# Performance work log

Hardware: AMD Instinct MI355X
Metric: run time of the kernel (lower is better)

Reference implementation:

```python
import jax, jax.numpy as jnp
import numpy as np

N_VOXELS = 400_000
FEAT_DIM = 128
BATCH = 4
NY = 512
NX = 512


def setup_inputs() -> dict:
    key = jax.random.key(0)
    k_feat, k_b, k_y, k_x = jax.random.split(key, 4)
    voxel_feat = jax.random.normal(k_feat, (N_VOXELS, FEAT_DIM), dtype=jnp.float32)
    b = jax.random.randint(k_b, (N_VOXELS,), 0, BATCH, dtype=jnp.int64 if jax.config.jax_enable_x64 else jnp.int32)
    z = jnp.zeros((N_VOXELS,), dtype=b.dtype)
    y = jax.random.randint(k_y, (N_VOXELS,), 0, NY, dtype=b.dtype)
    x = jax.random.randint(k_x, (N_VOXELS,), 0, NX, dtype=b.dtype)
    coors = jnp.stack([b, z, y, x], axis=1)  # [N, 4] = (batch, z, y, x)
    return {"voxel_feat": voxel_feat, "coors": coors, "batch_size": BATCH, "ny": NY, "nx": NX}


def reference(voxel_feat, coors, batch_size, ny, nx):
    # Fused equivalent of the per-batch python loop in _window2bev_old:
    # one flat scatter into a [B*ny*nx, C] canvas, then reshape to BEV layout.
    feat_dim = voxel_feat.shape[-1]
    flat_idx = coors[:, 0] * (ny * nx) + coors[:, 2] * nx + coors[:, 3]  # [N]
    canvas = jnp.zeros((batch_size * ny * nx, feat_dim), dtype=voxel_feat.dtype)
    canvas = canvas.at[flat_idx].set(voxel_feat)
    # [B, ny, nx, C] -> [B, C, ny, nx] to match torch output
    return canvas.reshape(batch_size, ny, nx, feat_dim).transpose(0, 3, 1, 2)
```

## Files before the change

kernel.cpp:

```cpp
#include <hip/hip_runtime.h>

#define FEAT_C 128
#define NB     4
#define NYv    512
#define NXv    512

typedef float vfloat4 __attribute__((ext_vector_type(4)));

__global__ void scatter_ids(const int4* __restrict__ coors,
                            int* __restrict__ idx_map, int n) {
    int i = blockIdx.x * blockDim.x + threadIdx.x;
    if (i >= n) return;
    int4 c = coors[i];
    int flat = c.x * (NYv * NXv) + c.z * NXv + c.w;
    atomicMax(&idx_map[flat], i);
}

__global__ __launch_bounds__(256) void gather_bev(
        const float* __restrict__ feat,
        const int* __restrict__ idx_map,
        float* __restrict__ out) {
    __shared__ float tile[64 * FEAT_C];
    __shared__ int sv[64];

    const int bid  = blockIdx.x;
    const int xseg = bid & 7;
    const int y    = (bid >> 3) & (NYv - 1);
    const int b    = bid >> (3 + 9);
    const int tid  = threadIdx.x;

    const int pix_base = b * (NYv * NXv) + y * NXv + xseg * 64;
    if (tid < 64) sv[tid] = idx_map[pix_base + tid];
    __syncthreads();

    const int wave = tid >> 6;
    const int lane = tid & 63;
    const int half = lane >> 5;
    const int l    = lane & 31;
#pragma unroll
    for (int k = 0; k < 8; ++k) {
        const int p = wave * 16 + 2 * k + half;
        const int v = sv[p];
        vfloat4 f = {0.f, 0.f, 0.f, 0.f};
        if (v >= 0) {
            f = ((const vfloat4*)(feat + v * FEAT_C))[l];
        }
        const int sw   = 4 * ((p >> 2) & 7);
        const int word = p * FEAT_C + ((4 * l) ^ sw);
        *(vfloat4*)&tile[word] = f;
    }
    __syncthreads();

    const long plane = (long)NYv * NXv;
    float* out_base = out + (long)b * FEAT_C * plane + (long)y * NXv + xseg * 64;
#pragma unroll
    for (int it = 0; it < 8; ++it) {
        const int j  = it * 256 + tid;
        const int c  = j >> 4;
        const int m  = j & 15;
        const int i0 = m << 2;
        const int cs = c ^ (4 * (m & 7));
        vfloat4 r;
        r.x = tile[(i0 + 0) * FEAT_C + cs];
        r.y = tile[(i0 + 1) * FEAT_C + cs];
        r.z = tile[(i0 + 2) * FEAT_C + cs];
        r.w = tile[(i0 + 3) * FEAT_C + cs];
        __builtin_nontemporal_store(r, (vfloat4*)(out_base + (long)c * plane + i0));
    }
}

extern "C" void kernel_launch(void* const* d_in, const int* in_sizes, int n_in,
                              void* d_out, int out_size, void* d_ws, size_t ws_size,
                              hipStream_t stream) {
    const float* feat  = (const float*)d_in[0];
    const int*   coors = (const int*)d_in[1];
    const int n = in_sizes[1] / 4;

    int* idx_map = (int*)d_ws;
    const size_t map_bytes = (size_t)NB * NYv * NXv * sizeof(int);

    (void)hipMemsetAsync(idx_map, 0xFF, map_bytes, stream);

    scatter_ids<<<(n + 255) / 256, 256, 0, stream>>>(
        (const int4*)coors, idx_map, n);

    const int nblocks = NB * NYv * (NXv / 64);
    gather_bev<<<nblocks, 256, 0, stream>>>(feat, idx_map, (float*)d_out);
}
```

Before: 707.6 us.

## Retile BEV gather to full-row by 32-channel blocks, drop nontemporal stores

Each block now covers a full 512-pixel row for a 32-channel group instead of a 64-pixel segment across all 128 channels. Threads read 128-byte slices of each voxel feature row, and each output channel row is written as one contiguous 2KB run. Nontemporal stores are replaced by regular stores. Each feature row is now fetched by four different blocks, so the feature read pattern is more fragmented in exchange for longer contiguous writes.

```diff
diff --git a/kernel.cpp b/kernel.cpp
--- a/kernel.cpp
+++ b/kernel.cpp
@@ -4,6 +4,8 @@
 #define NB     4
 #define NYv    512
 #define NXv    512
+#define CG     32
+#define NCG    (FEAT_C / CG)
 
 typedef float vfloat4 __attribute__((ext_vector_type(4)));
 
@@ -16,56 +18,54 @@
     atomicMax(&idx_map[flat], i);
 }
 
-__global__ __launch_bounds__(256) void gather_bev(
+__global__ __launch_bounds__(512) void gather_bev(
         const float* __restrict__ feat,
         const int* __restrict__ idx_map,
         float* __restrict__ out) {
-    __shared__ float tile[64 * FEAT_C];
-    __shared__ int sv[64];
+    __shared__ float tile[NXv * CG];
+    __shared__ int sv[NXv];
 
-    const int bid  = blockIdx.x;
-    const int xseg = bid & 7;
-    const int y    = (bid >> 3) & (NYv - 1);
-    const int b    = bid >> (3 + 9);
-    const int tid  = threadIdx.x;
+    const int bid = blockIdx.x;
+    const int cg  = bid & (NCG - 1);
+    const int y   = (bid >> 2) & (NYv - 1);
+    const int b   = bid >> 11;
+    const int tid = threadIdx.x;
 
-    const int pix_base = b * (NYv * NXv) + y * NXv + xseg * 64;
-    if (tid < 64) sv[tid] = idx_map[pix_base + tid];
+    sv[tid] = idx_map[b * (NYv * NXv) + y * NXv + tid];
     __syncthreads();
 
     const int wave = tid >> 6;
     const int lane = tid & 63;
-    const int half = lane >> 5;
-    const int l    = lane & 31;
+    const int sub  = lane >> 3;
+    const int l8   = lane & 7;
 #pragma unroll
     for (int k = 0; k < 8; ++k) {
-        const int p = wave * 16 + 2 * k + half;
+        const int p = wave * 64 + k * 8 + sub;
         const int v = sv[p];
         vfloat4 f = {0.f, 0.f, 0.f, 0.f};
         if (v >= 0) {
-            f = ((const vfloat4*)(feat + v * FEAT_C))[l];
+            f = ((const vfloat4*)(feat + (size_t)v * FEAT_C + cg * CG))[l8];
         }
-        const int sw   = 4 * ((p >> 2) & 7);
-        const int word = p * FEAT_C + ((4 * l) ^ sw);
+        const int word = p * CG + ((4 * l8) ^ (4 * ((p >> 2) & 7)));
         *(vfloat4*)&tile[word] = f;
     }
     __syncthreads();
 
     const long plane = (long)NYv * NXv;
-    float* out_base = out + (long)b * FEAT_C * plane + (long)y * NXv + xseg * 64;
+    float* out_base = out + ((long)b * FEAT_C + cg * CG) * plane + (long)y * NXv;
 #pragma unroll
     for (int it = 0; it < 8; ++it) {
-        const int j  = it * 256 + tid;
-        const int c  = j >> 4;
-        const int m  = j & 15;
+        const int j  = it * 512 + tid;
+        const int c  = ((j >> 4) & 3) + 4 * (j >> 9);
+        const int m  = (j & 15) + 16 * ((j >> 6) & 7);
         const int i0 = m << 2;
         const int cs = c ^ (4 * (m & 7));
         vfloat4 r;
-        r.x = tile[(i0 + 0) * FEAT_C + cs];
-        r.y = tile[(i0 + 1) * FEAT_C + cs];
-        r.z = tile[(i0 + 2) * FEAT_C + cs];
-        r.w = tile[(i0 + 3) * FEAT_C + cs];
-        __builtin_nontemporal_store(r, (vfloat4*)(out_base + (long)c * plane + i0));
+        r.x = tile[(i0 + 0) * CG + cs];
+        r.y = tile[(i0 + 1) * CG + cs];
+        r.z = tile[(i0 + 2) * CG + cs];
+        r.w = tile[(i0 + 3) * CG + cs];
+        *(vfloat4*)(out_base + (long)c * plane + i0) = r;
     }
 }
 
@@ -84,6 +84,6 @@
     scatter_ids<<<(n + 255) / 256, 256, 0, stream>>>(
         (const int4*)coors, idx_map, n);
 
-    const int nblocks = NB * NYv * (NXv / 64);
-    gather_bev<<<nblocks, 256, 0, stream>>>(feat, idx_map, (float*)d_out);
+    const int nblocks = NB * NYv * NCG;
+    gather_bev<<<nblocks, 512, 0, stream>>>(feat, idx_map, (float*)d_out);
 }
```

Measured after the change: 742.1 us. 4.9% more time.

## Widen gather tile to 256 pixels per block with 1024 threads

Applied to the files above, without the earlier changes.

The gather/transpose kernel now handles 256 consecutive x pixels per block using 1024 threads and a 128KB shared-memory tile, instead of 64 pixels with 256 threads. The output write mapping is reorganized so each half-wave stores one channel across 128 contiguous pixels, producing longer contiguous row segments per channel in the NCHW output. The larger tile limits occupancy to about one block per CU because of LDS usage, and there are 4x fewer blocks.

```diff
diff --git a/kernel.cpp b/kernel.cpp
--- a/kernel.cpp
+++ b/kernel.cpp
@@ -4,6 +4,7 @@
 #define NB     4
 #define NYv    512
 #define NXv    512
+#define PX     256
 
 typedef float vfloat4 __attribute__((ext_vector_type(4)));
 
@@ -16,50 +17,50 @@
     atomicMax(&idx_map[flat], i);
 }
 
-__global__ __launch_bounds__(256) void gather_bev(
+__global__ __launch_bounds__(1024) void gather_bev(
         const float* __restrict__ feat,
         const int* __restrict__ idx_map,
         float* __restrict__ out) {
-    __shared__ float tile[64 * FEAT_C];
-    __shared__ int sv[64];
+    __shared__ float tile[PX * FEAT_C];
+    __shared__ int sv[PX];
 
-    const int bid  = blockIdx.x;
-    const int xseg = bid & 7;
-    const int y    = (bid >> 3) & (NYv - 1);
-    const int b    = bid >> (3 + 9);
-    const int tid  = threadIdx.x;
+    const int bid = blockIdx.x;
+    const int xh  = bid & 1;
+    const int y   = (bid >> 1) & (NYv - 1);
+    const int b   = bid >> 10;
+    const int tid = threadIdx.x;
 
-    const int pix_base = b * (NYv * NXv) + y * NXv + xseg * 64;
-    if (tid < 64) sv[tid] = idx_map[pix_base + tid];
+    if (tid < PX)
+        sv[tid] = idx_map[b * (NYv * NXv) + y * NXv + xh * PX + tid];
     __syncthreads();
 
     const int wave = tid >> 6;
     const int lane = tid & 63;
     const int half = lane >> 5;
     const int l    = lane & 31;
+    const int hw   = wave * 2 + half;
 #pragma unroll
     for (int k = 0; k < 8; ++k) {
-        const int p = wave * 16 + 2 * k + half;
+        const int p = hw * 8 + k;
         const int v = sv[p];
         vfloat4 f = {0.f, 0.f, 0.f, 0.f};
         if (v >= 0) {
-            f = ((const vfloat4*)(feat + v * FEAT_C))[l];
+            f = ((const vfloat4*)(feat + (size_t)v * FEAT_C))[l];
         }
-        const int sw   = 4 * ((p >> 2) & 7);
-        const int word = p * FEAT_C + ((4 * l) ^ sw);
+        const int word = p * FEAT_C + ((4 * l) ^ (4 * ((p >> 2) & 7)));
         *(vfloat4*)&tile[word] = f;
     }
     __syncthreads();
 
     const long plane = (long)NYv * NXv;
-    float* out_base = out + (long)b * FEAT_C * plane + (long)y * NXv + xseg * 64;
+    float* out_base = out + (long)b * FEAT_C * plane + (long)y * NXv + xh * PX;
 #pragma unroll
     for (int it = 0; it < 8; ++it) {
-        const int j  = it * 256 + tid;
-        const int c  = j >> 4;
-        const int m  = j & 15;
-        const int i0 = m << 2;
-        const int cs = c ^ (4 * (m & 7));
+        const int h2 = it & 1;
+        const int cp = it >> 1;
+        const int c  = cp * 32 + wave * 2 + half;
+        const int i0 = 4 * l + 128 * h2;
+        const int cs = c ^ (4 * (l & 7));
         vfloat4 r;
         r.x = tile[(i0 + 0) * FEAT_C + cs];
         r.y = tile[(i0 + 1) * FEAT_C + cs];
@@ -84,6 +85,6 @@
     scatter_ids<<<(n + 255) / 256, 256, 0, stream>>>(
         (const int4*)coors, idx_map, n);
 
-    const int nblocks = NB * NYv * (NXv / 64);
-    gather_bev<<<nblocks, 256, 0, stream>>>(feat, idx_map, (float*)d_out);
+    const int nblocks = NB * NYv * (NXv / PX);
+    gather_bev<<<nblocks, 1024, 0, stream>>>(feat, idx_map, (float*)d_out);
 }
```

New measurement: 700.4 us. About the same (-1.0%).
